# Performance work log

Measured on AMD Instinct MI355X. Metric: run time of the kernel, lower is better.

The kernel has to match this reference:

```python
import jax, jax.numpy as jnp
import numpy as np

N_HEADS = 16
NEG = jnp.float32(-2**15 + 1)  # matches torch condition constant


def setup_inputs() -> dict:
    key = jax.random.key(0)
    ks = jax.random.split(key, 7)
    B, N, D = 4, 2048, 1024
    return {
        "q": jax.random.normal(ks[0], (B, N, D), jnp.float32),
        "k": jax.random.normal(ks[1], (B, N, D), jnp.float32),
        "v": jax.random.normal(ks[2], (B, N, D), jnp.float32),
        "w_qkv": jax.random.normal(ks[3], (3 * D, 3 * D), jnp.float32) * 0.02,
        "b_qkv": jax.random.normal(ks[4], (3 * D,), jnp.float32) * 0.02,
        "w_out": jax.random.normal(ks[5], (D, D), jnp.float32) * 0.02,
        "b_out": jax.random.normal(ks[6], (D,), jnp.float32) * 0.02,
    }


def reference(q, k, v, w_qkv, b_qkv, w_out, b_out):
    B, N, D = q.shape
    h = N_HEADS
    d = D // h
    scale = jnp.float32(d ** 0.5)  # NOTE: original multiplies by sqrt(d_head)

    x = jnp.concatenate([q, k, v], axis=-1)              # (B, N, 3D)
    qkv = x @ w_qkv.T + b_qkv                             # (B, N, 3D)
    qh, kh, vh = jnp.split(qkv, 3, axis=-1)
    split_heads = lambda t: t.reshape(B, N, h, d).transpose(0, 2, 1, 3)  # (B,h,N,d)
    qh, kh, vh = split_heads(qh), split_heads(kh), split_heads(vh)

    scores = jnp.einsum('bhnd,bhmd->bhnm', qh, kh) * scale  # (B,h,N,N)
    causal = jnp.tril(jnp.ones((N, N), dtype=bool))
    scores = jnp.where(causal, scores, NEG)
    attn = jax.nn.softmax(scores, axis=-1)
    out = jnp.einsum('bhnm,bhmd->bhnd', attn, vh)           # (B,h,N,d)
    out = out.transpose(0, 2, 1, 3).reshape(B, N, D)
    return out @ w_out.T + b_out
```

## Files before the change

### kernel.cpp

```cpp
#include <hip/hip_runtime.h>
#include <hip/hip_bf16.h>

#define SEQ   2048
#define DIM   1024
#define HEADS 16
#define DH    64
#define MROWS 8192
#define K3    3072
#define NEGV  (-32767.0f)
#define SCALE 8.0f

typedef __attribute__((ext_vector_type(8))) short bf16x8;
typedef __attribute__((ext_vector_type(4))) float f32x4;

__device__ __forceinline__ short f2bf(float x) {
  union { float f; unsigned u; } v; v.f = x;
  unsigned r = v.u + 0x7FFF + ((v.u >> 16) & 1);
  return (short)(r >> 16);
}
__device__ __forceinline__ float bf2f(short s) {
  union { float f; unsigned u; } v; v.u = ((unsigned)(unsigned short)s) << 16;
  return v.f;
}
__device__ __forceinline__ void split1(float x, short& h, short& l) {
  h = f2bf(x);
  l = f2bf(x - bf2f(h));
}
__device__ __forceinline__ void cvt_split8(const float4 a, const float4 b,
                                           bf16x8& hi, bf16x8& lo) {
  const float f[8] = {a.x, a.y, a.z, a.w, b.x, b.y, b.z, b.w};
#pragma unroll
  for (int i = 0; i < 8; i++) {
    short h, l; split1(f[i], h, l);
    hi[i] = h; lo[i] = l;
  }
}

__device__ __forceinline__ void glds16(const void* g, void* l) {
  __builtin_amdgcn_global_load_lds(
      (const __attribute__((address_space(1))) void*)g,
      (__attribute__((address_space(3))) void*)l, 16, 0, 0);
}

__device__ __forceinline__ int sw(int row, int col) {
  return row * 64 + ((((col >> 3) ^ row) & 7) << 3) + (col & 7);
}

__global__ __launch_bounds__(256) void prep_x(
    const float* __restrict__ q, const float* __restrict__ k,
    const float* __restrict__ v,
    short* __restrict__ ah, short* __restrict__ al)
{
  const int n = MROWS * (K3 / 4);
  for (int i = blockIdx.x * 256 + threadIdx.x; i < n; i += gridDim.x * 256) {
    const int r  = i / 768;
    const int c4 = i - r * 768;
    const float* src = (c4 < 256) ? q : ((c4 < 512) ? k : v);
    const int cc = c4 & 255;
    const float4 f = *(const float4*)(src + ((size_t)r * 256 + cc) * 4);
    const float fa[4] = {f.x, f.y, f.z, f.w};
    short hi[4], lo[4];
#pragma unroll
    for (int e = 0; e < 4; ++e) split1(fa[e], hi[e], lo[e]);
    const size_t o = (size_t)r * K3 + c4 * 4;
    *(short4*)(ah + o) = make_short4(hi[0], hi[1], hi[2], hi[3]);
    *(short4*)(al + o) = make_short4(lo[0], lo[1], lo[2], lo[3]);
  }
}

__global__ __launch_bounds__(256) void prep_w(
    const float* __restrict__ w,
    short* __restrict__ bh, short* __restrict__ bl)
{
  const int n = (K3 * K3) / 4;
  for (int i = blockIdx.x * 256 + threadIdx.x; i < n; i += gridDim.x * 256) {
    const float4 f = ((const float4*)w)[i];
    const float fa[4] = {f.x, f.y, f.z, f.w};
    short hi[4], lo[4];
#pragma unroll
    for (int e = 0; e < 4; ++e) split1(fa[e], hi[e], lo[e]);
    ((short4*)bh)[i] = make_short4(hi[0], hi[1], hi[2], hi[3]);
    ((short4*)bl)[i] = make_short4(lo[0], lo[1], lo[2], lo[3]);
  }
}

__global__ __launch_bounds__(256) void prep_wo(
    const float* __restrict__ w,
    short* __restrict__ wb)
{
  const int n = (DIM * DIM) / 4;
  for (int i = blockIdx.x * 256 + threadIdx.x; i < n; i += gridDim.x * 256) {
    const float4 f = ((const float4*)w)[i];
    ((short4*)wb)[i] = make_short4(f2bf(f.x), f2bf(f.y), f2bf(f.z), f2bf(f.w));
  }
}

__device__ __forceinline__ void stage_half(const short* __restrict__ src,
                                           short* dst, int wv, int lane) {
#pragma unroll
  for (int e = 0; e < 2; ++e) {
    const int idx = (wv * 2 + e) * 512 + lane * 8;
    const int row = idx >> 6;
    const int cb  = (idx >> 3) & 7;
    const int cbs = (cb ^ row) & 7;
    glds16(src + (size_t)row * K3 + cbs * 8, dst + (wv * 2 + e) * 512);
  }
}

__global__ __launch_bounds__(512, 2) void qkv_gemm_8p(
    const short* __restrict__ Ah, const short* __restrict__ Al,
    const short* __restrict__ Bh, const short* __restrict__ Bl,
    const float* __restrict__ bqkv,
    short* __restrict__ qh, short* __restrict__ ql)
{
  __shared__ short L[2][4][8192];

  const int t    = threadIdx.x;
  const int lane = t & 63;
  const int wv   = t >> 6;
  const int wr   = wv >> 2;
  const int wc   = wv & 3;
  const int l15  = lane & 15;
  const int lq   = lane >> 4;

  const int w  = (blockIdx.x & 7) * 32 + (blockIdx.x >> 3);
  const int Mb = (w & 31) * 256;
  const int Nb = (w >> 5) * 256;
  const int nt = 144;

  auto tsrc = [&](int kt, int h) -> const short* {
    kt = (kt < nt - 1) ? kt : (nt - 1);
    const int seg = (kt >= 96) ? 2 : ((kt >= 48) ? 1 : 0);
    const int k0  = (kt - seg * 48) * 64;
    if (h < 2) {
      const short* Apl = (seg == 2) ? Al : Ah;
      return Apl + (size_t)(Mb + h * 128) * K3 + k0;
    }
    const short* Bpl = (seg == 1) ? Bl : Bh;
    return Bpl + (size_t)(Nb + (h - 2) * 128) * K3 + k0;
  };

  f32x4 acc[8][4];
#pragma unroll
  for (int i = 0; i < 8; i++)
#pragma unroll
    for (int j = 0; j < 4; j++) acc[i][j] = (f32x4){0.f, 0.f, 0.f, 0.f};

  stage_half(tsrc(0, 0), &L[0][0][0], wv, lane);
  stage_half(tsrc(0, 1), &L[0][1][0], wv, lane);
  stage_half(tsrc(0, 2), &L[0][2][0], wv, lane);
  stage_half(tsrc(0, 3), &L[0][3][0], wv, lane);
  stage_half(tsrc(1, 2), &L[1][2][0], wv, lane);
  stage_half(tsrc(1, 3), &L[1][3][0], wv, lane);
  asm volatile("s_waitcnt vmcnt(4)" ::: "memory");
  __builtin_amdgcn_s_barrier();

  bf16x8 bfr[4][2];

  for (int kp = 0; kp < nt; kp += 2) {
#pragma unroll
    for (int p = 0; p < 8; ++p) {
      const int buf = p >> 2;
      const int qtr = p & 3;
      const int mi0 = qtr * 2;

      if (qtr == 0) {
#pragma unroll
        for (int ni = 0; ni < 4; ++ni)
#pragma unroll
          for (int ks = 0; ks < 2; ++ks)
            bfr[ni][ks] = *(const bf16x8*)(
                &L[buf][2 + (wc >> 1)][sw((wc & 1) * 64 + ni * 16 + l15,
                                          ks * 32 + lq * 8)]);
      }
      bf16x8 afr[2][2];
#pragma unroll
      for (int m = 0; m < 2; ++m)
#pragma unroll
        for (int ks = 0; ks < 2; ++ks)
          afr[m][ks] = *(const bf16x8*)(
              &L[buf][wr][sw((mi0 + m) * 16 + l15, ks * 32 + lq * 8)]);

      {
        const int SB[8] = {1, 1, 0, 0, 0, 0, 1, 1};
        const int SH[8] = {0, 1, 2, 3, 0, 1, 2, 3};
        const int SD[8] = {1, 1, 2, 2, 2, 2, 3, 3};
        stage_half(tsrc(kp + SD[p], SH[p]), &L[SB[p]][SH[p]][0], wv, lane);
      }

      if (qtr == 3) asm volatile("s_waitcnt vmcnt(4)" ::: "memory");
      __builtin_amdgcn_s_barrier();
      asm volatile("s_waitcnt lgkmcnt(0)" ::: "memory");
      __builtin_amdgcn_sched_barrier(0);

      __builtin_amdgcn_s_setprio(1);
#pragma unroll
      for (int m = 0; m < 2; ++m)
#pragma unroll
        for (int ni = 0; ni < 4; ++ni)
#pragma unroll
          for (int ks = 0; ks < 2; ++ks)
            acc[mi0 + m][ni] = __builtin_amdgcn_mfma_f32_16x16x32_bf16(
                afr[m][ks], bfr[ni][ks], acc[mi0 + m][ni], 0, 0, 0);
      __builtin_amdgcn_s_setprio(0);
      __builtin_amdgcn_s_barrier();
    }
  }

#pragma unroll
  for (int ni = 0; ni < 4; ++ni) {
    const int col = Nb + wc * 64 + ni * 16 + l15;
    const float bias = bqkv[col];
#pragma unroll
    for (int mi = 0; mi < 8; ++mi) {
#pragma unroll
      for (int r = 0; r < 4; ++r) {
        const int row = Mb + wr * 128 + mi * 16 + lq * 4 + r;
        const float xv = acc[mi][ni][r] + bias;
        const short hh = f2bf(xv);
        qh[(size_t)row * K3 + col] = hh;
        ql[(size_t)row * K3 + col] = f2bf(xv - bf2f(hh));
      }
    }
  }

  asm volatile("s_waitcnt vmcnt(0)" ::: "memory");
  __builtin_amdgcn_s_barrier();

  const int lt  = blockIdx.x >> 1;
  const int MbL = (lt & 31) * 256 + (blockIdx.x & 1) * 128;
  const int NbL = 2 * DIM + (lt >> 5) * 256;

  auto tsrcL = [&](int kt, int h) -> const short* {
    kt = (kt < 47) ? kt : 47;
    const int k0 = kt * 64;
    if (h == 0) return Ah + (size_t)MbL * K3 + k0;
    return Bh + (size_t)(NbL + (h - 2) * 128) * K3 + k0;
  };

#pragma unroll
  for (int i = 0; i < 4; i++)
#pragma unroll
    for (int j = 0; j < 4; j++) acc[i][j] = (f32x4){0.f, 0.f, 0.f, 0.f};

  stage_half(tsrcL(0, 0), &L[0][0][0], wv, lane);
  stage_half(tsrcL(0, 2), &L[0][2][0], wv, lane);
  stage_half(tsrcL(0, 3), &L[0][3][0], wv, lane);
  stage_half(tsrcL(1, 2), &L[1][2][0], wv, lane);
  stage_half(tsrcL(1, 3), &L[1][3][0], wv, lane);
  asm volatile("s_waitcnt vmcnt(4)" ::: "memory");
  __builtin_amdgcn_s_barrier();

  for (int kp = 0; kp < 48; kp += 2) {
#pragma unroll
    for (int p = 0; p < 4; ++p) {
      const int buf = p >> 1;
      const int mh  = p & 1;

      if (mh == 0) {
#pragma unroll
        for (int ni = 0; ni < 4; ++ni)
#pragma unroll
          for (int ks = 0; ks < 2; ++ks)
            bfr[ni][ks] = *(const bf16x8*)(
                &L[buf][2 + (wc >> 1)][sw((wc & 1) * 64 + ni * 16 + l15,
                                          ks * 32 + lq * 8)]);
      }
      bf16x8 afr[2][2];
#pragma unroll
      for (int m = 0; m < 2; ++m)
#pragma unroll
        for (int ks = 0; ks < 2; ++ks)
          afr[m][ks] = *(const bf16x8*)(
              &L[buf][0][sw(wr * 64 + (mh * 2 + m) * 16 + l15,
                            ks * 32 + lq * 8)]);

      if (p == 0) {
        stage_half(tsrcL(kp + 1, 0), &L[1][0][0], wv, lane);
      } else if (p == 1) {
        stage_half(tsrcL(kp + 2, 2), &L[0][2][0], wv, lane);
        stage_half(tsrcL(kp + 2, 3), &L[0][3][0], wv, lane);
      } else if (p == 2) {
        stage_half(tsrcL(kp + 2, 0), &L[0][0][0], wv, lane);
      } else {
        stage_half(tsrcL(kp + 3, 2), &L[1][2][0], wv, lane);
        stage_half(tsrcL(kp + 3, 3), &L[1][3][0], wv, lane);
      }

      if (mh == 1) asm volatile("s_waitcnt vmcnt(4)" ::: "memory");
      __builtin_amdgcn_s_barrier();
      asm volatile("s_waitcnt lgkmcnt(0)" ::: "memory");
      __builtin_amdgcn_sched_barrier(0);

      __builtin_amdgcn_s_setprio(1);
#pragma unroll
      for (int m = 0; m < 2; ++m)
#pragma unroll
        for (int ni = 0; ni < 4; ++ni)
#pragma unroll
          for (int ks = 0; ks < 2; ++ks)
            acc[mh * 2 + m][ni] = __builtin_amdgcn_mfma_f32_16x16x32_bf16(
                afr[m][ks], bfr[ni][ks], acc[mh * 2 + m][ni], 0, 0, 0);
      __builtin_amdgcn_s_setprio(0);
      __builtin_amdgcn_s_barrier();
    }
  }

#pragma unroll
  for (int ni = 0; ni < 4; ++ni) {
    const int col = NbL + wc * 64 + ni * 16 + l15;
    const float bias = bqkv[col];
#pragma unroll
    for (int mi = 0; mi < 4; ++mi) {
#pragma unroll
      for (int r = 0; r < 4; ++r) {
        const int row = MbL + wr * 64 + mi * 16 + lq * 4 + r;
        qh[(size_t)row * K3 + col] = f2bf(acc[mi][ni][r] + bias);
      }
    }
  }
}

__global__ __launch_bounds__(256) void qkv_gemm_fly(
    const float* __restrict__ q,
    const float* __restrict__ k,
    const float* __restrict__ v,
    const float* __restrict__ wqkv,
    const float* __restrict__ bqkv,
    short* __restrict__ qh, short* __restrict__ ql)
{
  __shared__ short Ash[128 * 32];
  __shared__ short Asl[128 * 32];
  __shared__ short Bsh[128 * 32];
  __shared__ short Bsl[128 * 32];

  const int t    = threadIdx.x;
  const int lane = t & 63;
  const int wv   = t >> 6;
  const int Mb   = blockIdx.y * 128;
  const int Nb   = blockIdx.x * 128;
  const bool prec = (Nb < 2 * DIM);
  const int wr   = (wv >> 1) * 64;
  const int wc   = (wv & 1) * 64;
  const int l15  = lane & 15;
  const int lq   = lane >> 4;
  const int srow = wv * 16 + (lane >> 2);
  const int scol = (lane & 3) * 8;

  f32x4 acc[4][4];
#pragma unroll
  for (int i = 0; i < 4; i++)
#pragma unroll
    for (int j = 0; j < 4; j++) acc[i][j] = (f32x4){0.f, 0.f, 0.f, 0.f};

  for (int k0 = 0; k0 < K3; k0 += 32) {
    const float* src = (k0 < DIM) ? q : ((k0 < 2 * DIM) ? k : v);
    const int koff = (k0 & (DIM - 1)) + scol;

    bf16x8 ah[2], al[2], bh[2], bl[2];
#pragma unroll
    for (int it = 0; it < 2; ++it) {
      const float* ap = src + (size_t)(Mb + it * 64 + srow) * DIM + koff;
      cvt_split8(*(const float4*)(ap), *(const float4*)(ap + 4), ah[it], al[it]);
      const float* bp = wqkv + (size_t)(Nb + it * 64 + srow) * K3 + k0 + scol;
      cvt_split8(*(const float4*)(bp), *(const float4*)(bp + 4), bh[it], bl[it]);
    }
    __syncthreads();
#pragma unroll
    for (int it = 0; it < 2; ++it) {
      *(bf16x8*)(Ash + (it * 64 + srow) * 32 + scol) = ah[it];
      *(bf16x8*)(Bsh + (it * 64 + srow) * 32 + scol) = bh[it];
      if (prec) {
        *(bf16x8*)(Asl + (it * 64 + srow) * 32 + scol) = al[it];
        *(bf16x8*)(Bsl + (it * 64 + srow) * 32 + scol) = bl[it];
      }
    }
    __syncthreads();

    bf16x8 afh[4], bfh[4];
#pragma unroll
    for (int i = 0; i < 4; i++)
      afh[i] = *(const bf16x8*)(Ash + (wr + i * 16 + l15) * 32 + lq * 8);
#pragma unroll
    for (int j = 0; j < 4; j++)
      bfh[j] = *(const bf16x8*)(Bsh + (wc + j * 16 + l15) * 32 + lq * 8);
#pragma unroll
    for (int i = 0; i < 4; i++)
#pragma unroll
      for (int j = 0; j < 4; j++)
        acc[i][j] = __builtin_amdgcn_mfma_f32_16x16x32_bf16(afh[i], bfh[j], acc[i][j], 0, 0, 0);

    if (prec) {
      bf16x8 afl[4], bfl[4];
#pragma unroll
      for (int i = 0; i < 4; i++)
        afl[i] = *(const bf16x8*)(Asl + (wr + i * 16 + l15) * 32 + lq * 8);
#pragma unroll
      for (int j = 0; j < 4; j++)
        bfl[j] = *(const bf16x8*)(Bsl + (wc + j * 16 + l15) * 32 + lq * 8);
#pragma unroll
      for (int i = 0; i < 4; i++)
#pragma unroll
        for (int j = 0; j < 4; j++) {
          acc[i][j] = __builtin_amdgcn_mfma_f32_16x16x32_bf16(afh[i], bfl[j], acc[i][j], 0, 0, 0);
          acc[i][j] = __builtin_amdgcn_mfma_f32_16x16x32_bf16(afl[i], bfh[j], acc[i][j], 0, 0, 0);
        }
    }
  }

#pragma unroll
  for (int j = 0; j < 4; j++) {
    const int col = Nb + wc + j * 16 + l15;
    const float bias = bqkv[col];
#pragma unroll
    for (int i = 0; i < 4; i++) {
#pragma unroll
      for (int r = 0; r < 4; r++) {
        const int row = Mb + wr + i * 16 + lq * 4 + r;
        const float xv = acc[i][j][r] + bias;
        const short hh = f2bf(xv);
        qh[(size_t)row * K3 + col] = hh;
        if (prec) ql[(size_t)row * K3 + col] = f2bf(xv - bf2f(hh));
      }
    }
  }
}

__global__ __launch_bounds__(512, 4) void attn_fwd(
    const short* __restrict__ qkvh,
    const short* __restrict__ qkvl,
    __hip_bfloat16* __restrict__ attno)
{
  __shared__ short Kh[2][4096], Kl[2][4096], Vt[2][4096];
  __shared__ short Ps[8][1024];

  const int bx = blockIdx.x;
  const int g  = bx >> 6;
  const int bh = bx & 63;
  const int h  = bh & 15;
  const int b  = bh >> 4;

  const int t    = threadIdx.x;
  const int lane = t & 63;
  const int wv   = t >> 6;
  const int l15  = lane & 15;
  const int quad = lane >> 4;
  const size_t rowBase = (size_t)b * SEQ;

  const short* gkbase = ((wv < 4) ? qkvh : qkvl) + DIM + h * DH;
  const int kw = wv & 3;
  const int vkey = t >> 3;
  const int vdb  = (t & 7) * 8;

#pragma unroll 1
  for (int pass = 0; pass < 2; ++pass) {
    const int qt = pass ? g : (15 - g);
    const int qb = qt * 128;

    bf16x8 qah[2], qal[2];
    {
      const size_t qoff = (rowBase + qb + 16 * wv + l15) * K3 + h * DH;
#pragma unroll
      for (int ks = 0; ks < 2; ++ks) {
        qah[ks] = *(const bf16x8*)(qkvh + qoff + ks * 32 + quad * 8);
        qal[ks] = *(const bf16x8*)(qkvl + qoff + ks * 32 + quad * 8);
#pragma unroll
        for (int e = 0; e < 8; ++e) {
          qah[ks][e] = f2bf(SCALE * bf2f(qah[ks][e]));
          qal[ks][e] = f2bf(SCALE * bf2f(qal[ks][e]));
        }
      }
    }

    float m_i[4], l_i[4];
    f32x4 O[4];
#pragma unroll
    for (int r = 0; r < 4; ++r) { m_i[r] = -1e30f; l_i[r] = 0.f; }
#pragma unroll
    for (int jd = 0; jd < 4; ++jd) O[jd] = (f32x4){0.f, 0.f, 0.f, 0.f};

    const int nkt = 2 * qt + 2;
    bf16x8 vreg;

    {
      const short* gk = gkbase + rowBase * K3;
      short* Kdst = (wv < 4) ? &Kh[0][0] : &Kl[0][0];
#pragma unroll
      for (int it = 0; it < 2; ++it) {
        const int row = kw * 16 + it * 8 + (lane >> 3);
        const int blk = ((lane & 7) ^ row) & 7;
        glds16(gk + (size_t)row * K3 + blk * 8, Kdst + (kw * 16 + it * 8) * 64);
      }
      vreg = *(const bf16x8*)(qkvh + (rowBase + vkey) * K3 + 2 * DIM + h * DH + vdb);
#pragma unroll
      for (int e = 0; e < 8; ++e) Vt[0][sw(vdb + e, vkey)] = vreg[e];
      asm volatile("s_waitcnt vmcnt(0)" ::: "memory");
    }
    __syncthreads();

    for (int kt = 0; kt < nkt; ++kt) {
      const int kb = kt * 64;
      const int cb = kt & 1;
      const bool more = (kt + 1 < nkt);

      if (more) {
        const short* gk = gkbase + (rowBase + kb + 64) * K3;
        short* Kdst = (wv < 4) ? &Kh[cb ^ 1][0] : &Kl[cb ^ 1][0];
#pragma unroll
        for (int it = 0; it < 2; ++it) {
          const int row = kw * 16 + it * 8 + (lane >> 3);
          const int blk = ((lane & 7) ^ row) & 7;
          glds16(gk + (size_t)row * K3 + blk * 8, Kdst + (kw * 16 + it * 8) * 64);
        }
        vreg = *(const bf16x8*)(qkvh + (rowBase + kb + 64 + vkey) * K3 +
                                2 * DIM + h * DH + vdb);
      }

      const bool active = (kb <= qb + 16 * wv + 15);

      if (active) {
        f32x4 s[4];
#pragma unroll
        for (int j = 0; j < 4; ++j) s[j] = (f32x4){0.f, 0.f, 0.f, 0.f};
        __builtin_amdgcn_s_setprio(1);
#pragma unroll
        for (int j = 0; j < 4; ++j) {
#pragma unroll
          for (int ks = 0; ks < 2; ++ks) {
            const bf16x8 kh = *(const bf16x8*)(&Kh[cb][sw(16 * j + l15, ks * 32 + quad * 8)]);
            const bf16x8 kl = *(const bf16x8*)(&Kl[cb][sw(16 * j + l15, ks * 32 + quad * 8)]);
            s[j] = __builtin_amdgcn_mfma_f32_16x16x32_bf16(qah[ks], kh, s[j], 0, 0, 0);
            s[j] = __builtin_amdgcn_mfma_f32_16x16x32_bf16(qal[ks], kh, s[j], 0, 0, 0);
            s[j] = __builtin_amdgcn_mfma_f32_16x16x32_bf16(qah[ks], kl, s[j], 0, 0, 0);
          }
        }
        __builtin_amdgcn_s_setprio(0);

        const int qrow0 = qb + 16 * wv + 4 * quad;
        const bool needmask = (kb + 63 > qb + 16 * wv);
        float p[4][4];
        float mt[4] = {-1e30f, -1e30f, -1e30f, -1e30f};
        if (needmask) {
#pragma unroll
          for (int j = 0; j < 4; ++j) {
            const int key = kb + 16 * j + l15;
#pragma unroll
            for (int r = 0; r < 4; ++r) {
              float sv = s[j][r];
              if (key > qrow0 + r) sv = NEGV;
              p[j][r] = sv;
              mt[r] = fmaxf(mt[r], sv);
            }
          }
        } else {
#pragma unroll
          for (int j = 0; j < 4; ++j)
#pragma unroll
            for (int r = 0; r < 4; ++r) {
              p[j][r] = s[j][r];
              mt[r] = fmaxf(mt[r], s[j][r]);
            }
        }
#pragma unroll
        for (int r = 0; r < 4; ++r) {
          mt[r] = fmaxf(mt[r], __shfl_xor(mt[r], 1));
          mt[r] = fmaxf(mt[r], __shfl_xor(mt[r], 2));
          mt[r] = fmaxf(mt[r], __shfl_xor(mt[r], 4));
          mt[r] = fmaxf(mt[r], __shfl_xor(mt[r], 8));
        }
        float alpha[4];
#pragma unroll
        for (int r = 0; r < 4; ++r) {
          const float mn = fmaxf(m_i[r], mt[r]);
          alpha[r] = __expf(m_i[r] - mn);
          m_i[r] = mn;
        }
        float ls[4] = {0.f, 0.f, 0.f, 0.f};
#pragma unroll
        for (int j = 0; j < 4; ++j)
#pragma unroll
          for (int r = 0; r < 4; ++r) {
            const float pe = __expf(p[j][r] - m_i[r]);
            ls[r] += pe;
            Ps[wv][sw(4 * quad + r, 16 * j + l15)] = f2bf(pe);
          }
#pragma unroll
        for (int r = 0; r < 4; ++r) {
          ls[r] += __shfl_xor(ls[r], 1);
          ls[r] += __shfl_xor(ls[r], 2);
          ls[r] += __shfl_xor(ls[r], 4);
          ls[r] += __shfl_xor(ls[r], 8);
          l_i[r] = l_i[r] * alpha[r] + ls[r];
        }
#pragma unroll
        for (int jd = 0; jd < 4; ++jd)
#pragma unroll
          for (int r = 0; r < 4; ++r) O[jd][r] *= alpha[r];

        __builtin_amdgcn_s_setprio(1);
#pragma unroll
        for (int ks = 0; ks < 2; ++ks) {
          const bf16x8 pa = *(const bf16x8*)(&Ps[wv][sw(l15, ks * 32 + quad * 8)]);
#pragma unroll
          for (int jd = 0; jd < 4; ++jd) {
            const bf16x8 vb = *(const bf16x8*)(&Vt[cb][sw(16 * jd + l15, ks * 32 + quad * 8)]);
            O[jd] = __builtin_amdgcn_mfma_f32_16x16x32_bf16(pa, vb, O[jd], 0, 0, 0);
          }
        }
        __builtin_amdgcn_s_setprio(0);
      }

      if (more) {
        asm volatile("s_waitcnt vmcnt(0)" ::: "memory");
#pragma unroll
        for (int e = 0; e < 8; ++e) Vt[cb ^ 1][sw(vdb + e, vkey)] = vreg[e];
      }
      __syncthreads();
    }

#pragma unroll
    for (int jd = 0; jd < 4; ++jd) {
#pragma unroll
      for (int r = 0; r < 4; ++r) {
        const int row = qb + 16 * wv + 4 * quad + r;
        attno[(rowBase + row) * DIM + h * DH + 16 * jd + l15] =
            __float2bfloat16(O[jd][r] / l_i[r]);
      }
    }
  }
}

__global__ __launch_bounds__(256) void out_gemm_pre(
    const short* __restrict__ a,
    const short* __restrict__ wob,
    const float* __restrict__ bo,
    float* __restrict__ out)
{
  __shared__ short As[128 * 32];
  __shared__ short Bs[128 * 32];

  const int t    = threadIdx.x;
  const int lane = t & 63;
  const int wv   = t >> 6;
  const int Mb   = blockIdx.y * 128;
  const int Nb   = blockIdx.x * 128;
  const int wr   = (wv >> 1) * 64;
  const int wc   = (wv & 1) * 64;
  const int l15  = lane & 15;
  const int lq   = lane >> 4;
  const int grow = lane >> 2;
  const int gcol = (lane & 3) * 8;

  f32x4 acc[4][4];
#pragma unroll
  for (int i = 0; i < 4; i++)
#pragma unroll
    for (int j = 0; j < 4; j++) acc[i][j] = (f32x4){0.f, 0.f, 0.f, 0.f};

  for (int k0 = 0; k0 < DIM; k0 += 32) {
    __syncthreads();
#pragma unroll
    for (int it = 0; it < 2; ++it) {
      const int r0 = wv * 32 + it * 16;
      glds16(a   + (size_t)(Mb + r0 + grow) * DIM + k0 + gcol, As + r0 * 32);
      glds16(wob + (size_t)(Nb + r0 + grow) * DIM + k0 + gcol, Bs + r0 * 32);
    }
    __syncthreads();

    bf16x8 af[4], bfr[4];
#pragma unroll
    for (int i = 0; i < 4; i++)
      af[i] = *(const bf16x8*)(As + (wr + i * 16 + l15) * 32 + lq * 8);
#pragma unroll
    for (int j = 0; j < 4; j++)
      bfr[j] = *(const bf16x8*)(Bs + (wc + j * 16 + l15) * 32 + lq * 8);
#pragma unroll
    for (int i = 0; i < 4; i++)
#pragma unroll
      for (int j = 0; j < 4; j++)
        acc[i][j] = __builtin_amdgcn_mfma_f32_16x16x32_bf16(af[i], bfr[j], acc[i][j], 0, 0, 0);
  }

#pragma unroll
  for (int j = 0; j < 4; j++) {
    const int col = Nb + wc + j * 16 + l15;
    const float bias = bo[col];
#pragma unroll
    for (int i = 0; i < 4; i++) {
#pragma unroll
      for (int r = 0; r < 4; r++) {
        const int row = Mb + wr + i * 16 + lq * 4 + r;
        out[(size_t)row * DIM + col] = acc[i][j][r] + bias;
      }
    }
  }
}

__global__ __launch_bounds__(256) void out_gemm(
    const __hip_bfloat16* __restrict__ a,
    const float* __restrict__ wo,
    const float* __restrict__ bo,
    float* __restrict__ out)
{
  __shared__ short As[128 * 32];
  __shared__ short Bs[128 * 32];

  const int t    = threadIdx.x;
  const int lane = t & 63;
  const int wv   = t >> 6;
  const int Mb   = blockIdx.y * 128;
  const int Nb   = blockIdx.x * 128;
  const int wr   = (wv >> 1) * 64;
  const int wc   = (wv & 1) * 64;
  const int l15  = lane & 15;
  const int lq   = lane >> 4;
  const int srow = wv * 16 + (lane >> 2);
  const int scol = (lane & 3) * 8;

  f32x4 acc[4][4];
#pragma unroll
  for (int i = 0; i < 4; i++)
#pragma unroll
    for (int j = 0; j < 4; j++) acc[i][j] = (f32x4){0.f, 0.f, 0.f, 0.f};

  for (int k0 = 0; k0 < DIM; k0 += 32) {
    bf16x8 areg[2], breg[2];
#pragma unroll
    for (int it = 0; it < 2; ++it) {
      areg[it] = *(const bf16x8*)(a + (size_t)(Mb + it * 64 + srow) * DIM + k0 + scol);
      const float* bp = wo + (size_t)(Nb + it * 64 + srow) * DIM + k0 + scol;
      const float4 b0 = *(const float4*)(bp);
      const float4 b1 = *(const float4*)(bp + 4);
      const float bf8[8] = {b0.x, b0.y, b0.z, b0.w, b1.x, b1.y, b1.z, b1.w};
#pragma unroll
      for (int e = 0; e < 8; e++) breg[it][e] = f2bf(bf8[e]);
    }
    __syncthreads();
#pragma unroll
    for (int it = 0; it < 2; ++it) {
      *(bf16x8*)(As + (it * 64 + srow) * 32 + scol) = areg[it];
      *(bf16x8*)(Bs + (it * 64 + srow) * 32 + scol) = breg[it];
    }
    __syncthreads();

    bf16x8 af[4], bfr[4];
#pragma unroll
    for (int i = 0; i < 4; i++)
      af[i] = *(const bf16x8*)(As + (wr + i * 16 + l15) * 32 + lq * 8);
#pragma unroll
    for (int j = 0; j < 4; j++)
      bfr[j] = *(const bf16x8*)(Bs + (wc + j * 16 + l15) * 32 + lq * 8);
#pragma unroll
    for (int i = 0; i < 4; i++)
#pragma unroll
      for (int j = 0; j < 4; j++)
        acc[i][j] = __builtin_amdgcn_mfma_f32_16x16x32_bf16(af[i], bfr[j], acc[i][j], 0, 0, 0);
  }

#pragma unroll
  for (int j = 0; j < 4; j++) {
    const int col = Nb + wc + j * 16 + l15;
    const float bias = bo[col];
#pragma unroll
    for (int i = 0; i < 4; i++) {
#pragma unroll
      for (int r = 0; r < 4; r++) {
        const int row = Mb + wr + i * 16 + lq * 4 + r;
        out[(size_t)row * DIM + col] = acc[i][j][r] + bias;
      }
    }
  }
}

extern "C" void kernel_launch(void* const* d_in, const int* in_sizes, int n_in,
                              void* d_out, int out_size, void* d_ws, size_t ws_size,
                              hipStream_t stream) {
  const float* q    = (const float*)d_in[0];
  const float* k    = (const float*)d_in[1];
  const float* v    = (const float*)d_in[2];
  const float* wqkv = (const float*)d_in[3];
  const float* bqkv = (const float*)d_in[4];
  const float* wout = (const float*)d_in[5];
  const float* bout = (const float*)d_in[6];

  const size_t PLANE = (size_t)MROWS * K3 * 2;
  const size_t BPLN  = (size_t)K3 * K3 * 2;
  short* qh = (short*)d_ws;
  short* ql = (short*)((char*)d_ws + PLANE);
  char*  p2 = (char*)d_ws + 2 * PLANE;
  __hip_bfloat16* attnws = (__hip_bfloat16*)p2;

  const size_t NEED = 2 * PLANE + 2 * PLANE + 2 * BPLN;

  if (ws_size >= NEED) {
    short* Ah = (short*)p2;
    short* Al = Ah + (size_t)MROWS * K3;
    short* Bh = Al + (size_t)MROWS * K3;
    short* Bl = Bh + (size_t)K3 * K3;
    short* wob = (short*)(p2 + (size_t)MROWS * DIM * 2);
    prep_x<<<4096, 256, 0, stream>>>(q, k, v, Ah, Al);
    prep_w<<<2048, 256, 0, stream>>>(wqkv, Bh, Bl);
    qkv_gemm_8p<<<dim3(256), 512, 0, stream>>>(Ah, Al, Bh, Bl, bqkv, qh, ql);
    prep_wo<<<256, 256, 0, stream>>>(wout, wob);
    attn_fwd<<<dim3(512), 512, 0, stream>>>(qh, ql, attnws);
    out_gemm_pre<<<dim3(DIM / 128, MROWS / 128), 256, 0, stream>>>(
        (const short*)attnws, wob, bout, (float*)d_out);
  } else {
    qkv_gemm_fly<<<dim3(K3 / 128, MROWS / 128), 256, 0, stream>>>(
        q, k, v, wqkv, bqkv, qh, ql);
    attn_fwd<<<dim3(512), 512, 0, stream>>>(qh, ql, attnws);
    out_gemm<<<dim3(DIM / 128, MROWS / 128), 256, 0, stream>>>(attnws, wout, bout,
                                                               (float*)d_out);
  }
}
```

Before: 672.7 us.

## Merge prep kernels into one launch and skip softmax rescale when max unchanged

Combines the three input/weight conversion kernels into a single grid-stride kernel, placing the bf16 output-weight buffer in extra workspace when available so it can be converted early. In the attention loop, rescaling of the running sum and output accumulators is skipped when no row's running max grows (wave-uniform check via __any). This removes two kernel launches and some per-tile multiplies and exps, at the cost of a branch and divergence-free vote, and it relies on the workspace being large enough for the early path.

```diff
diff --git a/kernel.cpp b/kernel.cpp
--- a/kernel.cpp
+++ b/kernel.cpp
@@ -46,41 +46,46 @@
   return row * 64 + ((((col >> 3) ^ row) & 7) << 3) + (col & 7);
 }
 
-__global__ __launch_bounds__(256) void prep_x(
+__global__ __launch_bounds__(256) void prep_all(
     const float* __restrict__ q, const float* __restrict__ k,
-    const float* __restrict__ v,
-    short* __restrict__ ah, short* __restrict__ al)
+    const float* __restrict__ v, const float* __restrict__ w,
+    const float* __restrict__ wo,
+    short* __restrict__ ah, short* __restrict__ al,
+    short* __restrict__ bh, short* __restrict__ bl,
+    short* __restrict__ wob, int do_wo)
 {
-  const int n = MROWS * (K3 / 4);
+  const int nx  = MROWS * (K3 / 4);
+  const int nw  = (K3 * K3) / 4;
+  const int nwo = do_wo ? (DIM * DIM) / 4 : 0;
+  const int n   = nx + nw + nwo;
   for (int i = blockIdx.x * 256 + threadIdx.x; i < n; i += gridDim.x * 256) {
-    const int r  = i / 768;
-    const int c4 = i - r * 768;
-    const float* src = (c4 < 256) ? q : ((c4 < 512) ? k : v);
-    const int cc = c4 & 255;
-    const float4 f = *(const float4*)(src + ((size_t)r * 256 + cc) * 4);
-    const float fa[4] = {f.x, f.y, f.z, f.w};
-    short hi[4], lo[4];
-#pragma unroll
-    for (int e = 0; e < 4; ++e) split1(fa[e], hi[e], lo[e]);
-    const size_t o = (size_t)r * K3 + c4 * 4;
-    *(short4*)(ah + o) = make_short4(hi[0], hi[1], hi[2], hi[3]);
-    *(short4*)(al + o) = make_short4(lo[0], lo[1], lo[2], lo[3]);
-  }
-}
-
-__global__ __launch_bounds__(256) void prep_w(
-    const float* __restrict__ w,
-    short* __restrict__ bh, short* __restrict__ bl)
-{
-  const int n = (K3 * K3) / 4;
-  for (int i = blockIdx.x * 256 + threadIdx.x; i < n; i += gridDim.x * 256) {
-    const float4 f = ((const float4*)w)[i];
-    const float fa[4] = {f.x, f.y, f.z, f.w};
-    short hi[4], lo[4];
-#pragma unroll
-    for (int e = 0; e < 4; ++e) split1(fa[e], hi[e], lo[e]);
-    ((short4*)bh)[i] = make_short4(hi[0], hi[1], hi[2], hi[3]);
-    ((short4*)bl)[i] = make_short4(lo[0], lo[1], lo[2], lo[3]);
+    if (i < nx) {
+      const int r  = i / 768;
+      const int c4 = i - r * 768;
+      const float* src = (c4 < 256) ? q : ((c4 < 512) ? k : v);
+      const int cc = c4 & 255;
+      const float4 f = *(const float4*)(src + ((size_t)r * 256 + cc) * 4);
+      const float fa[4] = {f.x, f.y, f.z, f.w};
+      short hi[4], lo[4];
+#pragma unroll
+      for (int e = 0; e < 4; ++e) split1(fa[e], hi[e], lo[e]);
+      const size_t o = (size_t)r * K3 + c4 * 4;
+      *(short4*)(ah + o) = make_short4(hi[0], hi[1], hi[2], hi[3]);
+      *(short4*)(al + o) = make_short4(lo[0], lo[1], lo[2], lo[3]);
+    } else if (i < nx + nw) {
+      const int j = i - nx;
+      const float4 f = ((const float4*)w)[j];
+      const float fa[4] = {f.x, f.y, f.z, f.w};
+      short hi[4], lo[4];
+#pragma unroll
+      for (int e = 0; e < 4; ++e) split1(fa[e], hi[e], lo[e]);
+      ((short4*)bh)[j] = make_short4(hi[0], hi[1], hi[2], hi[3]);
+      ((short4*)bl)[j] = make_short4(lo[0], lo[1], lo[2], lo[3]);
+    } else {
+      const int j = i - nx - nw;
+      const float4 f = ((const float4*)wo)[j];
+      ((short4*)wob)[j] = make_short4(f2bf(f.x), f2bf(f.y), f2bf(f.z), f2bf(f.w));
+    }
   }
 }
 
@@ -568,12 +573,17 @@
           mt[r] = fmaxf(mt[r], __shfl_xor(mt[r], 4));
           mt[r] = fmaxf(mt[r], __shfl_xor(mt[r], 8));
         }
+
+        const bool grow = __any(mt[0] > m_i[0] || mt[1] > m_i[1] ||
+                                mt[2] > m_i[2] || mt[3] > m_i[3]);
         float alpha[4];
-#pragma unroll
-        for (int r = 0; r < 4; ++r) {
-          const float mn = fmaxf(m_i[r], mt[r]);
-          alpha[r] = __expf(m_i[r] - mn);
-          m_i[r] = mn;
+        if (grow) {
+#pragma unroll
+          for (int r = 0; r < 4; ++r) {
+            const float mn = fmaxf(m_i[r], mt[r]);
+            alpha[r] = __expf(m_i[r] - mn);
+            m_i[r] = mn;
+          }
         }
         float ls[4] = {0.f, 0.f, 0.f, 0.f};
 #pragma unroll
@@ -590,12 +600,18 @@
           ls[r] += __shfl_xor(ls[r], 2);
           ls[r] += __shfl_xor(ls[r], 4);
           ls[r] += __shfl_xor(ls[r], 8);
-          l_i[r] = l_i[r] * alpha[r] + ls[r];
-        }
-#pragma unroll
-        for (int jd = 0; jd < 4; ++jd)
-#pragma unroll
-          for (int r = 0; r < 4; ++r) O[jd][r] *= alpha[r];
+        }
+        if (grow) {
+#pragma unroll
+          for (int r = 0; r < 4; ++r) l_i[r] = l_i[r] * alpha[r] + ls[r];
+#pragma unroll
+          for (int jd = 0; jd < 4; ++jd)
+#pragma unroll
+            for (int r = 0; r < 4; ++r) O[jd][r] *= alpha[r];
+        } else {
+#pragma unroll
+          for (int r = 0; r < 4; ++r) l_i[r] += ls[r];
+        }
 
         __builtin_amdgcn_s_setprio(1);
 #pragma unroll
@@ -785,6 +801,7 @@
 
   const size_t PLANE = (size_t)MROWS * K3 * 2;
   const size_t BPLN  = (size_t)K3 * K3 * 2;
+  const size_t WOB   = (size_t)DIM * DIM * 2;
   short* qh = (short*)d_ws;
   short* ql = (short*)((char*)d_ws + PLANE);
   char*  p2 = (char*)d_ws + 2 * PLANE;
@@ -797,11 +814,13 @@
     short* Al = Ah + (size_t)MROWS * K3;
     short* Bh = Al + (size_t)MROWS * K3;
     short* Bl = Bh + (size_t)K3 * K3;
-    short* wob = (short*)(p2 + (size_t)MROWS * DIM * 2);
-    prep_x<<<4096, 256, 0, stream>>>(q, k, v, Ah, Al);
-    prep_w<<<2048, 256, 0, stream>>>(wqkv, Bh, Bl);
+    const bool woEarly = (ws_size >= NEED + WOB);
+    short* wob = woEarly ? (short*)((char*)d_ws + NEED)
+                         : (short*)(p2 + (size_t)MROWS * DIM * 2);
+    prep_all<<<4096, 256, 0, stream>>>(q, k, v, wqkv, wout,
+                                       Ah, Al, Bh, Bl, wob, woEarly ? 1 : 0);
     qkv_gemm_8p<<<dim3(256), 512, 0, stream>>>(Ah, Al, Bh, Bl, bqkv, qh, ql);
-    prep_wo<<<256, 256, 0, stream>>>(wout, wob);
+    if (!woEarly) prep_wo<<<256, 256, 0, stream>>>(wout, wob);
     attn_fwd<<<dim3(512), 512, 0, stream>>>(qh, ql, attnws);
     out_gemm_pre<<<dim3(DIM / 128, MROWS / 128), 256, 0, stream>>>(
         (const short*)attnws, wob, bout, (float*)d_out);
```

After: 698.1 us. 1.04x slower.
